# Kernel optimization log

Measured on AMD Instinct MI355X. Metric: run time of the kernel, lower is better.

The kernel has to match this reference:

```python
import jax, jax.numpy as jnp
import numpy as np

N_NODES = 100000
N_EDGES = 800000
D_EDGE = 64
D_NODE = 128
D_OUT = 128


def setup_inputs() -> dict:
    key = jax.random.key(0)
    ks = jax.random.split(key, 7)
    vdata = jax.random.normal(ks[0], (N_NODES, D_NODE), dtype=jnp.float32)
    edata_a = jax.random.normal(ks[1], (N_EDGES, D_EDGE), dtype=jnp.float32)
    edata_b = jax.random.normal(ks[2], (N_EDGES, D_EDGE), dtype=jnp.float32)
    conn_a = jax.random.randint(ks[3], (2, N_EDGES), 0, N_NODES, dtype=jnp.int64)
    conn_b = jax.random.randint(ks[4], (2, N_EDGES), 0, N_NODES, dtype=jnp.int64)
    d_in = 2 * D_EDGE + D_NODE  # aggregated (per-type) concat + vdata
    W = jax.random.normal(ks[5], (d_in, D_OUT), dtype=jnp.float32) / np.sqrt(d_in)
    b = jnp.zeros((D_OUT,), dtype=jnp.float32)
    return {"vdata": vdata, "edata_a": edata_a, "edata_b": edata_b,
            "conn_a": conn_a, "conn_b": conn_b, "W": W, "b": b}


def _aggregate(edata, receivers, num_nodes):
    # scatter-sum edge features into node-sized buffer (Aggregator with sum reduce)
    return jax.ops.segment_sum(edata, receivers, num_segments=num_nodes)


def reference(vdata, edata_a, edata_b, conn_a, conn_b, W, b):
    n = vdata.shape[0]
    agg_a = _aggregate(edata_a, conn_a[1, :], n)  # [N, D_EDGE]
    agg_b = _aggregate(edata_b, conn_b[1, :], n)  # [N, D_EDGE]
    x = jnp.concatenate([agg_a, agg_b, vdata], axis=1)  # [N, 2*D_EDGE + D_NODE]
    return x @ W + b  # dense updater (Linear)
```

## Files before the change

kernel.cpp:

```cpp
#include <hip/hip_runtime.h>


#define EDGES_PER_WAVE 8
#define NB 32

__global__ __launch_bounds__(256) void scatter_kernel(
    const float* __restrict__ edata, const int* __restrict__ recv,
    float* __restrict__ agg, int n_edges) {
  const int lane = threadIdx.x & 63;
  const int wave = blockIdx.x * (blockDim.x >> 6) + (threadIdx.x >> 6);
  const int e0 = wave * EDGES_PER_WAVE;

  if (e0 + EDGES_PER_WAVE <= n_edges) {
    int r[EDGES_PER_WAVE];
    float v[EDGES_PER_WAVE];
#pragma unroll
    for (int i = 0; i < EDGES_PER_WAVE; ++i) {
      const int e = e0 + i;
      r[i] = recv[e];
      v[i] = edata[(size_t)e * 64 + lane];
    }
#pragma unroll
    for (int i = 0; i < EDGES_PER_WAVE; ++i) {
      atomicAdd(&agg[(size_t)r[i] * 64 + lane], v[i]);
    }
  } else {
    for (int e = e0; e < n_edges; ++e) {
      const int r = recv[e];
      const float v = edata[(size_t)e * 64 + lane];
      atomicAdd(&agg[(size_t)r * 64 + lane], v);
    }
  }
}

__device__ __forceinline__ void fma4(float4& acc, float s, const float4& w) {
  acc.x = fmaf(s, w.x, acc.x);
  acc.y = fmaf(s, w.y, acc.y);
  acc.z = fmaf(s, w.z, acc.z);
  acc.w = fmaf(s, w.w, acc.w);
}

__global__ __launch_bounds__(256) void fused_gemm_kernel(
    const float* __restrict__ agg_a, const float* __restrict__ agg_b,
    const float* __restrict__ vdata, const float* __restrict__ W,
    const float* __restrict__ bias, float* __restrict__ out, int n_nodes) {
  __shared__ float xs[NB][260];

  const int tid = threadIdx.x;
  const int n0 = blockIdx.x * NB;

  const float4* A4 = (const float4*)(agg_a + (size_t)n0 * 64);
  const float4* B4 = (const float4*)(agg_b + (size_t)n0 * 64);
  const float4* V4 = (const float4*)(vdata + (size_t)n0 * 128);
#pragma unroll
  for (int i = tid; i < NB * 16; i += 256) {
    const int node = i >> 4;
    const int kk = (i & 15) << 2;
    *(float4*)&xs[node][kk] = A4[i];
    *(float4*)&xs[node][64 + kk] = B4[i];
  }
#pragma unroll
  for (int i = tid; i < NB * 32; i += 256) {
    const int node = i >> 5;
    const int kk = (i & 31) << 2;
    *(float4*)&xs[node][128 + kk] = V4[i];
  }
  __syncthreads();

  const int c = tid & 31;
  const int nset = tid >> 5;
  const float4* W4 = (const float4*)W;

  float4 acc0 = {0.f, 0.f, 0.f, 0.f};
  float4 acc1 = acc0, acc2 = acc0, acc3 = acc0;

#pragma unroll 4
  for (int k = 0; k < 256; k += 4) {
    const float4 w0 = W4[(k + 0) * 32 + c];
    const float4 w1 = W4[(k + 1) * 32 + c];
    const float4 w2 = W4[(k + 2) * 32 + c];
    const float4 w3 = W4[(k + 3) * 32 + c];
    const float4 x0 = *(const float4*)&xs[nset * 4 + 0][k];
    const float4 x1 = *(const float4*)&xs[nset * 4 + 1][k];
    const float4 x2 = *(const float4*)&xs[nset * 4 + 2][k];
    const float4 x3 = *(const float4*)&xs[nset * 4 + 3][k];

    fma4(acc0, x0.x, w0); fma4(acc0, x0.y, w1); fma4(acc0, x0.z, w2); fma4(acc0, x0.w, w3);
    fma4(acc1, x1.x, w0); fma4(acc1, x1.y, w1); fma4(acc1, x1.z, w2); fma4(acc1, x1.w, w3);
    fma4(acc2, x2.x, w0); fma4(acc2, x2.y, w1); fma4(acc2, x2.z, w2); fma4(acc2, x2.w, w3);
    fma4(acc3, x3.x, w0); fma4(acc3, x3.y, w1); fma4(acc3, x3.z, w2); fma4(acc3, x3.w, w3);
  }

  const float4 bb = ((const float4*)bias)[c];
  acc0.x += bb.x; acc0.y += bb.y; acc0.z += bb.z; acc0.w += bb.w;
  acc1.x += bb.x; acc1.y += bb.y; acc1.z += bb.z; acc1.w += bb.w;
  acc2.x += bb.x; acc2.y += bb.y; acc2.z += bb.z; acc2.w += bb.w;
  acc3.x += bb.x; acc3.y += bb.y; acc3.z += bb.z; acc3.w += bb.w;

  float4* O4 = (float4*)out;
  const int nb = n0 + nset * 4;
  if (nb + 3 < n_nodes) {
    O4[(size_t)(nb + 0) * 32 + c] = acc0;
    O4[(size_t)(nb + 1) * 32 + c] = acc1;
    O4[(size_t)(nb + 2) * 32 + c] = acc2;
    O4[(size_t)(nb + 3) * 32 + c] = acc3;
  } else {
    if (nb + 0 < n_nodes) O4[(size_t)(nb + 0) * 32 + c] = acc0;
    if (nb + 1 < n_nodes) O4[(size_t)(nb + 1) * 32 + c] = acc1;
    if (nb + 2 < n_nodes) O4[(size_t)(nb + 2) * 32 + c] = acc2;
    if (nb + 3 < n_nodes) O4[(size_t)(nb + 3) * 32 + c] = acc3;
  }
}

extern "C" void kernel_launch(void* const* d_in, const int* in_sizes, int n_in,
                              void* d_out, int out_size, void* d_ws, size_t ws_size,
                              hipStream_t stream) {
  const float* vdata   = (const float*)d_in[0];
  const float* edata_a = (const float*)d_in[1];
  const float* edata_b = (const float*)d_in[2];
  const int*   conn_a  = (const int*)d_in[3];
  const int*   conn_b  = (const int*)d_in[4];
  const float* W       = (const float*)d_in[5];
  const float* bias    = (const float*)d_in[6];
  float*       out     = (float*)d_out;

  const int n_nodes = in_sizes[0] / 128;
  const int n_edges = in_sizes[1] / 64;

  float* agg_a = (float*)d_ws;
  float* agg_b = agg_a + (size_t)n_nodes * 64;

  hipMemsetAsync(d_ws, 0, (size_t)n_nodes * 64 * 2 * sizeof(float), stream);

  const int waves = (n_edges + EDGES_PER_WAVE - 1) / EDGES_PER_WAVE;
  const int sblocks = (waves + 3) / 4;
  scatter_kernel<<<sblocks, 256, 0, stream>>>(edata_a, conn_a + n_edges, agg_a, n_edges);
  scatter_kernel<<<sblocks, 256, 0, stream>>>(edata_b, conn_b + n_edges, agg_b, n_edges);

  const int gblocks = (n_nodes + NB - 1) / NB;
  fused_gemm_kernel<<<gblocks, 256, 0, stream>>>(agg_a, agg_b, vdata, W, bias, out, n_nodes);
}
```

Measured before the change: 780.5 us.

## Replace atomic edge scatter with CSR build and per-node gather reduction

```diff
diff --git a/kernel.cpp b/kernel.cpp
--- a/kernel.cpp
+++ b/kernel.cpp
@@ -1,36 +1,131 @@
 #include <hip/hip_runtime.h>
 
 
-#define EDGES_PER_WAVE 8
-#define NB 32
-
-__global__ __launch_bounds__(256) void scatter_kernel(
-    const float* __restrict__ edata, const int* __restrict__ recv,
-    float* __restrict__ agg, int n_edges) {
+#define NB 64
+
+__global__ __launch_bounds__(256) void hist_kernel(
+    const int* __restrict__ recv_a, const int* __restrict__ recv_b,
+    int* __restrict__ counts, int E, int N) {
+  const int i = blockIdx.x * 256 + threadIdx.x;
+  if (i >= 2 * E) return;
+  const int t = (i >= E);
+  const int e = t ? i - E : i;
+  const int r = t ? recv_b[e] : recv_a[e];
+  atomicAdd(&counts[t * N + r], 1);
+}
+
+__global__ __launch_bounds__(256) void scan_s1(
+    const int* __restrict__ counts, int* __restrict__ row_start,
+    int* __restrict__ block_sums, int n) {
+  __shared__ int sdata[256];
+  const int t = threadIdx.x;
+  const int i0 = blockIdx.x * 1024 + t * 4;
+  int c0 = 0, c1 = 0, c2 = 0, c3 = 0;
+  if (i0 + 3 < n) {
+    const int4 v = *(const int4*)&counts[i0];
+    c0 = v.x; c1 = v.y; c2 = v.z; c3 = v.w;
+  } else {
+    if (i0 + 0 < n) c0 = counts[i0 + 0];
+    if (i0 + 1 < n) c1 = counts[i0 + 1];
+    if (i0 + 2 < n) c2 = counts[i0 + 2];
+    if (i0 + 3 < n) c3 = counts[i0 + 3];
+  }
+  const int s = c0 + c1 + c2 + c3;
+  sdata[t] = s;
+  __syncthreads();
+  int v = s;
+  for (int d = 1; d < 256; d <<= 1) {
+    const int add = (t >= d) ? sdata[t - d] : 0;
+    __syncthreads();
+    v += add;
+    sdata[t] = v;
+    __syncthreads();
+  }
+  const int excl = v - s;
+  if (i0 + 0 < n) row_start[i0 + 0] = excl;
+  if (i0 + 1 < n) row_start[i0 + 1] = excl + c0;
+  if (i0 + 2 < n) row_start[i0 + 2] = excl + c0 + c1;
+  if (i0 + 3 < n) row_start[i0 + 3] = excl + c0 + c1 + c2;
+  if (t == 255) block_sums[blockIdx.x] = v;
+}
+
+__global__ __launch_bounds__(256) void scan_s2(
+    int* __restrict__ block_sums, int* __restrict__ row_start,
+    int nblocks, int n, int total) {
+  __shared__ int sdata[256];
+  const int t = threadIdx.x;
+  const int s = (t < nblocks) ? block_sums[t] : 0;
+  sdata[t] = s;
+  __syncthreads();
+  int v = s;
+  for (int d = 1; d < 256; d <<= 1) {
+    const int add = (t >= d) ? sdata[t - d] : 0;
+    __syncthreads();
+    v += add;
+    sdata[t] = v;
+    __syncthreads();
+  }
+  if (t < nblocks) block_sums[t] = v - s;
+  if (t == 0) row_start[n] = total;
+}
+
+__global__ __launch_bounds__(256) void scan_s3(
+    int* __restrict__ row_start, int* __restrict__ cursor,
+    const int* __restrict__ block_sums, int n) {
+  const int i0 = blockIdx.x * 1024 + threadIdx.x * 4;
+  const int off = block_sums[blockIdx.x];
+#pragma unroll
+  for (int j = 0; j < 4; ++j) {
+    if (i0 + j < n) {
+      const int v = row_start[i0 + j] + off;
+      row_start[i0 + j] = v;
+      cursor[i0 + j] = v;
+    }
+  }
+}
+
+__global__ __launch_bounds__(256) void fill_kernel(
+    const int* __restrict__ recv_a, const int* __restrict__ recv_b,
+    int* __restrict__ cursor, int* __restrict__ perm, int E, int N) {
+  const int i = blockIdx.x * 256 + threadIdx.x;
+  if (i >= 2 * E) return;
+  const int t = (i >= E);
+  const int e = t ? i - E : i;
+  const int r = t ? recv_b[e] : recv_a[e];
+  const int pos = atomicAdd(&cursor[t * N + r], 1);
+  perm[pos] = e;
+}
+
+__global__ __launch_bounds__(256) void gather_kernel(
+    const float* __restrict__ edata_a, const float* __restrict__ edata_b,
+    const int* __restrict__ perm, const int* __restrict__ row_start,
+    float* __restrict__ agg_a, float* __restrict__ agg_b, int N) {
+  const int w = blockIdx.x * 4 + (threadIdx.x >> 6);
+  if (w >= 2 * N) return;
   const int lane = threadIdx.x & 63;
-  const int wave = blockIdx.x * (blockDim.x >> 6) + (threadIdx.x >> 6);
-  const int e0 = wave * EDGES_PER_WAVE;
-
-  if (e0 + EDGES_PER_WAVE <= n_edges) {
-    int r[EDGES_PER_WAVE];
-    float v[EDGES_PER_WAVE];
-#pragma unroll
-    for (int i = 0; i < EDGES_PER_WAVE; ++i) {
-      const int e = e0 + i;
-      r[i] = recv[e];
-      v[i] = edata[(size_t)e * 64 + lane];
-    }
-#pragma unroll
-    for (int i = 0; i < EDGES_PER_WAVE; ++i) {
-      atomicAdd(&agg[(size_t)r[i] * 64 + lane], v[i]);
-    }
-  } else {
-    for (int e = e0; e < n_edges; ++e) {
-      const int r = recv[e];
-      const float v = edata[(size_t)e * 64 + lane];
-      atomicAdd(&agg[(size_t)r * 64 + lane], v);
-    }
-  }
+  const int t = (w >= N);
+  const int n = t ? w - N : w;
+  const int start = row_start[w];
+  const int end = row_start[w + 1];
+  const float* __restrict__ ed = t ? edata_b : edata_a;
+  float* __restrict__ ag = t ? agg_b : agg_a;
+  const int g = lane >> 4;
+  const int fo = (lane & 15) << 2;
+
+  float4 acc = {0.f, 0.f, 0.f, 0.f};
+  for (int j = start + g; j < end; j += 4) {
+    const int e = perm[j];
+    const float4 v = *(const float4*)(ed + (size_t)e * 64 + fo);
+    acc.x += v.x; acc.y += v.y; acc.z += v.z; acc.w += v.w;
+  }
+#pragma unroll
+  for (int m = 16; m <= 32; m <<= 1) {
+    acc.x += __shfl_xor(acc.x, m);
+    acc.y += __shfl_xor(acc.y, m);
+    acc.z += __shfl_xor(acc.z, m);
+    acc.w += __shfl_xor(acc.w, m);
+  }
+  if (g == 0) *(float4*)(ag + (size_t)n * 64 + fo) = acc;
 }
 
 __device__ __forceinline__ void fma4(float4& acc, float s, const float4& w) {
@@ -48,22 +143,26 @@
 
   const int tid = threadIdx.x;
   const int n0 = blockIdx.x * NB;
+  const int nvalid = min(NB, n_nodes - n0);
 
   const float4* A4 = (const float4*)(agg_a + (size_t)n0 * 64);
   const float4* B4 = (const float4*)(agg_b + (size_t)n0 * 64);
   const float4* V4 = (const float4*)(vdata + (size_t)n0 * 128);
+  const int limAB = nvalid * 16, limV = nvalid * 32;
+  const float4 z4 = {0.f, 0.f, 0.f, 0.f};
+
 #pragma unroll
   for (int i = tid; i < NB * 16; i += 256) {
     const int node = i >> 4;
     const int kk = (i & 15) << 2;
-    *(float4*)&xs[node][kk] = A4[i];
-    *(float4*)&xs[node][64 + kk] = B4[i];
+    *(float4*)&xs[node][kk]      = (i < limAB) ? A4[i] : z4;
+    *(float4*)&xs[node][64 + kk] = (i < limAB) ? B4[i] : z4;
   }
 #pragma unroll
   for (int i = tid; i < NB * 32; i += 256) {
     const int node = i >> 5;
     const int kk = (i & 31) << 2;
-    *(float4*)&xs[node][128 + kk] = V4[i];
+    *(float4*)&xs[node][128 + kk] = (i < limV) ? V4[i] : z4;
   }
   __syncthreads();
 
@@ -71,44 +170,34 @@
   const int nset = tid >> 5;
   const float4* W4 = (const float4*)W;
 
-  float4 acc0 = {0.f, 0.f, 0.f, 0.f};
-  float4 acc1 = acc0, acc2 = acc0, acc3 = acc0;
-
-#pragma unroll 4
+  float4 acc[8] = {};
+
+#pragma unroll 2
   for (int k = 0; k < 256; k += 4) {
     const float4 w0 = W4[(k + 0) * 32 + c];
     const float4 w1 = W4[(k + 1) * 32 + c];
     const float4 w2 = W4[(k + 2) * 32 + c];
     const float4 w3 = W4[(k + 3) * 32 + c];
-    const float4 x0 = *(const float4*)&xs[nset * 4 + 0][k];
-    const float4 x1 = *(const float4*)&xs[nset * 4 + 1][k];
-    const float4 x2 = *(const float4*)&xs[nset * 4 + 2][k];
-    const float4 x3 = *(const float4*)&xs[nset * 4 + 3][k];
-
-    fma4(acc0, x0.x, w0); fma4(acc0, x0.y, w1); fma4(acc0, x0.z, w2); fma4(acc0, x0.w, w3);
-    fma4(acc1, x1.x, w0); fma4(acc1, x1.y, w1); fma4(acc1, x1.z, w2); fma4(acc1, x1.w, w3);
-    fma4(acc2, x2.x, w0); fma4(acc2, x2.y, w1); fma4(acc2, x2.z, w2); fma4(acc2, x2.w, w3);
-    fma4(acc3, x3.x, w0); fma4(acc3, x3.y, w1); fma4(acc3, x3.z, w2); fma4(acc3, x3.w, w3);
+#pragma unroll
+    for (int nn = 0; nn < 8; ++nn) {
+      const float4 x = *(const float4*)&xs[nset * 8 + nn][k];
+      fma4(acc[nn], x.x, w0);
+      fma4(acc[nn], x.y, w1);
+      fma4(acc[nn], x.z, w2);
+      fma4(acc[nn], x.w, w3);
+    }
   }
 
   const float4 bb = ((const float4*)bias)[c];
-  acc0.x += bb.x; acc0.y += bb.y; acc0.z += bb.z; acc0.w += bb.w;
-  acc1.x += bb.x; acc1.y += bb.y; acc1.z += bb.z; acc1.w += bb.w;
-  acc2.x += bb.x; acc2.y += bb.y; acc2.z += bb.z; acc2.w += bb.w;
-  acc3.x += bb.x; acc3.y += bb.y; acc3.z += bb.z; acc3.w += bb.w;
-
   float4* O4 = (float4*)out;
-  const int nb = n0 + nset * 4;
-  if (nb + 3 < n_nodes) {
-    O4[(size_t)(nb + 0) * 32 + c] = acc0;
-    O4[(size_t)(nb + 1) * 32 + c] = acc1;
-    O4[(size_t)(nb + 2) * 32 + c] = acc2;
-    O4[(size_t)(nb + 3) * 32 + c] = acc3;
-  } else {
-    if (nb + 0 < n_nodes) O4[(size_t)(nb + 0) * 32 + c] = acc0;
-    if (nb + 1 < n_nodes) O4[(size_t)(nb + 1) * 32 + c] = acc1;
-    if (nb + 2 < n_nodes) O4[(size_t)(nb + 2) * 32 + c] = acc2;
-    if (nb + 3 < n_nodes) O4[(size_t)(nb + 3) * 32 + c] = acc3;
+#pragma unroll
+  for (int nn = 0; nn < 8; ++nn) {
+    const int node = n0 + nset * 8 + nn;
+    if (node < n_nodes) {
+      float4 r = acc[nn];
+      r.x += bb.x; r.y += bb.y; r.z += bb.z; r.w += bb.w;
+      O4[(size_t)node * 32 + c] = r;
+    }
   }
 }
 
@@ -124,19 +213,37 @@
   const float* bias    = (const float*)d_in[6];
   float*       out     = (float*)d_out;
 
-  const int n_nodes = in_sizes[0] / 128;
-  const int n_edges = in_sizes[1] / 64;
-
-  float* agg_a = (float*)d_ws;
-  float* agg_b = agg_a + (size_t)n_nodes * 64;
-
-  hipMemsetAsync(d_ws, 0, (size_t)n_nodes * 64 * 2 * sizeof(float), stream);
-
-  const int waves = (n_edges + EDGES_PER_WAVE - 1) / EDGES_PER_WAVE;
-  const int sblocks = (waves + 3) / 4;
-  scatter_kernel<<<sblocks, 256, 0, stream>>>(edata_a, conn_a + n_edges, agg_a, n_edges);
-  scatter_kernel<<<sblocks, 256, 0, stream>>>(edata_b, conn_b + n_edges, agg_b, n_edges);
-
-  const int gblocks = (n_nodes + NB - 1) / NB;
-  fused_gemm_kernel<<<gblocks, 256, 0, stream>>>(agg_a, agg_b, vdata, W, bias, out, n_nodes);
-}
+  const int N = in_sizes[0] / 128;
+  const int E = in_sizes[1] / 64;
+
+  const int* recv_a = conn_a + E;
+  const int* recv_b = conn_b + E;
+
+  float* agg_a     = (float*)d_ws;
+  float* agg_b     = agg_a + (size_t)N * 64;
+  int*   perm      = (int*)(agg_b + (size_t)N * 64);
+  int*   counts    = perm + 2 * (size_t)E;
+  int*   row_start = counts + 2 * (size_t)N;
+  int*   cursor    = row_start + 2 * (size_t)N + 1;
+  int*   block_sums = cursor + 2 * (size_t)N;
+
+  hipMemsetAsync(counts, 0, 2 * (size_t)N * sizeof(int), stream);
+
+  const int eblocks = (2 * E + 255) / 256;
+  hist_kernel<<<eblocks, 256, 0, stream>>>(recv_a, recv_b, counts, E, N);
+
+  const int n2 = 2 * N;
+  const int sblocks = (n2 + 1023) / 1024;
+  scan_s1<<<sblocks, 256, 0, stream>>>(counts, row_start, block_sums, n2);
+  scan_s2<<<1, 256, 0, stream>>>(block_sums, row_start, sblocks, n2, 2 * E);
+  scan_s3<<<sblocks, 256, 0, stream>>>(row_start, cursor, block_sums, n2);
+
+  fill_kernel<<<eblocks, 256, 0, stream>>>(recv_a, recv_b, cursor, perm, E, N);
+
+  const int gwaves = 2 * N;
+  gather_kernel<<<(gwaves + 3) / 4, 256, 0, stream>>>(
+      edata_a, edata_b, perm, row_start, agg_a, agg_b, N);
+
+  const int gblocks = (N + NB - 1) / NB;
+  fused_gemm_kernel<<<gblocks, 256, 0, stream>>>(agg_a, agg_b, vdata, W, bias, out, N);
+}
```

Result: no change. 783.3 us (+0.4%).
